# Kernel optimization log

Hardware: AMD Instinct MI355X
Metric: run time of the kernel (lower is better)

The kernel has to match this reference:

```python
import jax, jax.numpy as jnp
import numpy as np

N = 200000; S = 128; P = 4; K = 27
C_IN = 256; C_OUT = 256; N_IN = 64; N_OUT = 64
DILATIONS = [1, 3, 9, 27]
EPS = 1e-5


def _build_pairs():
    """Precompute (in_idx, out_idx) gather/scatter pairs per path & kernel offset,
    mimicking MinkowskiEngine's coordinate-hash-map kernel maps."""
    rng = np.random.default_rng(0)
    lin = rng.choice(S ** 3, size=N, replace=False)
    xs = lin // (S * S); ys = (lin // S) % S; zs = lin % S
    coords = np.stack([xs, ys, zs], axis=1).astype(np.int64)  # [N,3]
    order = np.argsort(lin)
    skeys = lin[order]
    offs = np.array([[dx, dy, dz] for dx in (-1, 0, 1) for dy in (-1, 0, 1) for dz in (-1, 0, 1)], dtype=np.int64)  # [27,3]
    pairs = [[None] * K for _ in range(P)]
    max_m = 1
    for p, d in enumerate(DILATIONS):
        for k in range(K):
            nc = coords + offs[k] * d  # neighbor coords for each output point
            valid = np.all((nc >= 0) & (nc < S), axis=1)
            idx_out = np.nonzero(valid)[0]
            nkey = (nc[valid, 0] * S + nc[valid, 1]) * S + nc[valid, 2]
            pos = np.searchsorted(skeys, nkey)
            pos_c = np.minimum(pos, N - 1)
            found = skeys[pos_c] == nkey
            j = order[pos_c[found]]       # source (input) point index
            i = idx_out[found]            # destination (output) point index
            pairs[p][k] = (j.astype(np.int32), i.astype(np.int32))
            max_m = max(max_m, len(j))
    in_idx = np.full((P, K, max_m), N, dtype=np.int32)   # sentinel N -> zero/dummy row
    out_idx = np.full((P, K, max_m), N, dtype=np.int32)
    for p in range(P):
        for k in range(K):
            j, i = pairs[p][k]
            in_idx[p, k, : len(j)] = j
            out_idx[p, k, : len(i)] = i
    return jnp.asarray(in_idx), jnp.asarray(out_idx)


def setup_inputs() -> dict:
    key = jax.random.key(0)
    ks = jax.random.split(key, 8)
    in_idx, out_idx = _build_pairs()
    x = jax.random.normal(ks[0], (N, C_IN), dtype=jnp.float32)
    Wl = jax.random.normal(ks[1], (P, C_IN, N_IN), dtype=jnp.float32) * (1.0 / np.sqrt(C_IN))
    bl = jax.random.normal(ks[2], (P, N_IN), dtype=jnp.float32) * 0.01
    Wc = jax.random.normal(ks[3], (P, K, N_IN, N_OUT), dtype=jnp.float32) * (1.0 / np.sqrt(K * N_IN))
    gamma = jnp.ones((P, N_OUT), dtype=jnp.float32)
    beta = jnp.zeros((P, N_OUT), dtype=jnp.float32)
    W2 = jax.random.normal(ks[4], (C_OUT, C_OUT), dtype=jnp.float32) * (1.0 / np.sqrt(C_OUT))
    b2 = jax.random.normal(ks[5], (C_OUT,), dtype=jnp.float32) * 0.01
    return {"x": x, "Wl": Wl, "bl": bl, "Wc": Wc, "gamma": gamma, "beta": beta,
            "W2": W2, "b2": b2, "in_idx": in_idx, "out_idx": out_idx}


def reference(x, Wl, bl, Wc, gamma, beta, W2, b2, in_idx, out_idx):
    n = x.shape[0]
    zero_row = jnp.zeros((1, N_IN), dtype=x.dtype)
    paths = []
    for p in range(P):  # fixed small cardinality loop (structurally distinct dilations)
        h = x @ Wl[p] + bl[p]                      # MinkowskiLinear: [N, nIn]
        hp = jnp.concatenate([h, zero_row], axis=0)  # dummy row for padded pairs
        g = hp[in_idx[p]]                          # gather: [K, M, nIn]
        c = jnp.einsum('kmc,kcd->kmd', g, Wc[p])   # per-offset matmul
        out = jnp.zeros((n + 1, N_OUT), dtype=x.dtype)
        out = out.at[out_idx[p].reshape(-1)].add(c.reshape(-1, N_OUT))[:n]  # scatter-add
        mu = out.mean(axis=0)
        var = jnp.mean((out - mu) ** 2, axis=0)    # biased var, as torch BN training mode
        out = (out - mu) * jax.lax.rsqrt(var + EPS) * gamma[p] + beta[p]
        paths.append(jax.nn.relu(out))
    cat = jnp.concatenate(paths, axis=-1)          # [N, out_features]
    return cat @ W2 + b2 + x                       # 1x1 linear + identity residual
```

## Files before the change

kernel.cpp:

```cpp
#include <hip/hip_runtime.h>
#include <hip/hip_bf16.h>

constexpr float EPS = 1e-5f;

typedef _Float16 f16x8 __attribute__((ext_vector_type(8)));
typedef __attribute__((ext_vector_type(4))) float floatx4;

__global__ __launch_bounds__(256) void k0_wct(
    const float* __restrict__ Wc, _Float16* __restrict__ wct)
{
    __shared__ float T[64][65];
    const int pk = blockIdx.x;
    const float* src = Wc + (size_t)pk * 4096;
    _Float16* dst = wct + (size_t)pk * 4096;
    const int t = threadIdx.x;
    #pragma unroll
    for (int e = 0; e < 16; e++) {
        const int idx = t + 256 * e;
        T[idx >> 6][idx & 63] = src[idx];
    }
    __syncthreads();
    #pragma unroll
    for (int e = 0; e < 16; e++) {
        const int idx = t + 256 * e;
        const int d = idx >> 6, q = idx & 63;
        const int sc = q >> 3, j = q & 7;
        const int cin = ((sc ^ (d & 7)) << 3) | j;
        dst[idx] = (_Float16)T[cin][d];
    }
}

__global__ __launch_bounds__(256) void k0_wlt(
    const float* __restrict__ Wl, _Float16* __restrict__ wlt)
{
    __shared__ float T[64][65];
    const int p = blockIdx.x, ct = blockIdx.y;
    const int t = threadIdx.x;
    #pragma unroll
    for (int e = 0; e < 16; e++) {
        const int idx = t + 256 * e;
        const int c = idx >> 6, d = idx & 63;
        T[c][d] = Wl[((size_t)p * 256 + ct * 64 + c) * 64 + d];
    }
    __syncthreads();
    #pragma unroll
    for (int e = 0; e < 16; e++) {
        const int idx = t + 256 * e;
        const int d = idx >> 6, c = idx & 63;
        wlt[((size_t)p * 64 + d) * 256 + ct * 64 + c] = (_Float16)T[c][d];
    }
}

__global__ __launch_bounds__(256) void k0_w2t(
    const float* __restrict__ W2, _Float16* __restrict__ w2t)
{
    __shared__ float T[64][65];
    const int kt = blockIdx.x, ct = blockIdx.y;
    const int t = threadIdx.x;
    #pragma unroll
    for (int e = 0; e < 16; e++) {
        const int idx = t + 256 * e;
        const int kk = idx >> 6, c = idx & 63;
        T[kk][c] = W2[((size_t)kt * 64 + kk) * 256 + ct * 64 + c];
    }
    __syncthreads();
    #pragma unroll
    for (int e = 0; e < 16; e++) {
        const int idx = t + 256 * e;
        const int c = idx >> 6, kk = idx & 63;
        w2t[((size_t)ct * 64 + c) * 256 + kt * 64 + kk] = (_Float16)T[kk][c];
    }
}

__global__ __launch_bounds__(512, 4) void k1_gemm_h(
    const float* __restrict__ x, const _Float16* __restrict__ wlt,
    const float* __restrict__ bl, _Float16* __restrict__ hb, int n)
{
    __shared__ __align__(16) _Float16 As[128 * 128];
    __shared__ __align__(16) _Float16 Bs[64 * 128];
    __shared__ float blS[256];

    const int row0 = blockIdx.x << 7;
    const int t    = threadIdx.x;
    const int lane = t & 63;
    const int wv   = t >> 6;
    const int mrow = lane & 15;
    const int quad = lane >> 4;

    if (t < 256) blS[t] = bl[t];

    floatx4 acc[4][4];
    #pragma unroll
    for (int a = 0; a < 4; a++)
        #pragma unroll
        for (int b = 0; b < 4; b++) acc[a][b] = floatx4{0.f, 0.f, 0.f, 0.f};

    #pragma unroll
    for (int kh = 0; kh < 2; kh++) {
        __syncthreads();
        #pragma unroll
        for (int i = 0; i < 4; i++) {
            const int cid = t + 512 * i;
            const int r = cid >> 4, ck = cid & 15;
            const int gr = row0 + r;
            f16x8 v;
            if (gr < n) {
                const float* g = x + (size_t)gr * 256 + kh * 128 + (ck << 3);
                const float4 f0 = *(const float4*)g;
                const float4 f1 = *(const float4*)(g + 4);
                v[0] = (_Float16)f0.x; v[1] = (_Float16)f0.y;
                v[2] = (_Float16)f0.z; v[3] = (_Float16)f0.w;
                v[4] = (_Float16)f1.x; v[5] = (_Float16)f1.y;
                v[6] = (_Float16)f1.z; v[7] = (_Float16)f1.w;
            } else {
                #pragma unroll
                for (int j = 0; j < 8; j++) v[j] = (_Float16)0.f;
            }
            *(f16x8*)&As[r * 128 + ((ck ^ (r & 7)) << 3)] = v;
        }
        #pragma unroll
        for (int cg = 0; cg < 4; cg++) {
            __syncthreads();
            #pragma unroll
            for (int it = 0; it < 2; it++) {
                const int lin = t + 512 * it;
                const int r = lin >> 4, sc = lin & 15;
                const _Float16* gs = wlt + (size_t)(cg * 64 + r) * 256
                                     + kh * 128 + ((sc ^ (r & 7)) << 3);
                __builtin_amdgcn_global_load_lds(
                    (const __attribute__((address_space(1))) void*)gs,
                    (__attribute__((address_space(3))) void*)((char*)Bs + lin * 16),
                    16, 0, 0);
            }
            __syncthreads();
            #pragma unroll
            for (int s = 0; s < 4; s++) {
                const int r = (wv << 4) + mrow;
                const f16x8 a = *(const f16x8*)&As[r * 128 + ((((s << 2) + quad) ^ (r & 7)) << 3)];
                #pragma unroll
                for (int tc = 0; tc < 4; tc++) {
                    const int rn = (tc << 4) + mrow;
                    const f16x8 b = *(const f16x8*)&Bs[rn * 128 + ((((s << 2) + quad) ^ (rn & 7)) << 3)];
                    acc[cg][tc] = __builtin_amdgcn_mfma_f32_16x16x32_f16(a, b, acc[cg][tc], 0, 0, 0);
                }
            }
        }
    }
    __syncthreads();
    #pragma unroll
    for (int cg = 0; cg < 4; cg++)
        #pragma unroll
        for (int tc = 0; tc < 4; tc++)
            #pragma unroll
            for (int rg = 0; rg < 4; rg++) {
                const int r = row0 + (wv << 4) + (quad << 2) + rg;
                const int c = (cg << 6) + (tc << 4) + mrow;
                if (r < n)
                    hb[(size_t)r * 256 + c] = (_Float16)(acc[cg][tc][rg] + blS[c]);
            }
}

__global__ __launch_bounds__(512) void k2_conv(
    const _Float16* __restrict__ hb, const _Float16* __restrict__ wct,
    const int* __restrict__ in_idx, const int* __restrict__ out_idx,
    float* __restrict__ accum, float* __restrict__ ssum,
    float* __restrict__ ssq, int n, int M)
{
    __shared__ __align__(16) _Float16 Ws[2][4096];
    __shared__ float Acc[128][66];
    __shared__ int csrc[2][128];
    __shared__ int cdst[2][128];
    __shared__ int spos_s[27];
    __shared__ int epos_s[27];

    const int p    = blockIdx.y;
    const int t    = threadIdx.x;
    const int lane = t & 63;
    const int wv   = t >> 6;
    const int mrow = lane & 15;
    const int quad = lane >> 4;

    const int nwg = gridDim.x;
    const int qq = nwg >> 3, rr = nwg & 7;
    const int xcd = blockIdx.x & 7, ii = blockIdx.x >> 3;
    const int bx = (xcd < rr ? xcd * (qq + 1) : rr * (qq + 1) + (xcd - rr) * qq) + ii;
    const int row0 = bx << 7;

    for (int i = t; i < 128 * 66; i += 512) ((float*)Acc)[i] = 0.0f;

    if (t < 54) {
        const int kk = (t < 27) ? t : t - 27;
        const int upper = (row0 + 128 > n) ? n : row0 + 128;
        const int target = (t < 27) ? row0 : upper;
        const int* oi = out_idx + (size_t)(p * 27 + kk) * M;
        int lo = 0, hi = M;
        while (lo < hi) {
            const int mid = (lo + hi) >> 1;
            if (oi[mid] < target) lo = mid + 1; else hi = mid;
        }
        if (t < 27) spos_s[kk] = lo; else epos_s[kk] = lo;
    }
    __syncthreads();

#define STAGE(buf, kk) do {                                                         \
        const char* gs_ = (const char*)wct + (((size_t)(p * 27 + (kk))) << 13)      \
                          + (wv << 10) + (lane << 4);                               \
        __builtin_amdgcn_global_load_lds(                                           \
            (const __attribute__((address_space(1))) void*)gs_,                     \
            (__attribute__((address_space(3))) void*)((char*)&Ws[buf][0] + (wv << 10)), \
            16, 0, 0);                                                              \
    } while (0)

#define COMPACT(buf, kk) do {                                                       \
        if (t < 128) {                                                              \
            const int sp_ = spos_s[kk];                                             \
            int cn_ = epos_s[kk] - sp_;                                             \
            if (cn_ > 128) cn_ = 128;                                               \
            const size_t base_ = (size_t)(p * 27 + (kk)) * M + sp_;                 \
            int v_ = n;                                                             \
            if (t < cn_) {                                                          \
                v_ = in_idx[base_ + t];                                             \
                cdst[buf][t] = out_idx[base_ + t] - row0;                           \
            }                                                                       \
            csrc[buf][t] = v_;                                                      \
        }                                                                           \
    } while (0)

    STAGE(0, 0);
    COMPACT(0, 0);
    __syncthreads();

    for (int k = 0; k < 27; k++) {
        const int cur = k & 1;
        if (k < 26) { STAGE(cur ^ 1, k + 1); COMPACT(cur ^ 1, k + 1); }

        int cnt = epos_s[k] - spos_s[k];
        if (cnt > 128) cnt = 128;
        const int tids = ((cnt + 15) >> 4) << 2;
        const int bsw  = (quad ^ (mrow & 7)) << 3;

        for (int tid = wv; tid < tids; tid += 8) {
            const int tr = tid >> 2, tc = tid & 3;
            const int srow = csrc[cur][(tr << 4) + mrow];
            const _Float16* ar = hb + ((size_t)srow << 8) + (p << 6) + (quad << 3);
            const f16x8 a0 = *(const f16x8*)ar;
            const f16x8 a1 = *(const f16x8*)(ar + 32);
            const int brow = ((tc << 4) + mrow) << 6;
            const f16x8 b0 = *(const f16x8*)(Ws[cur] + brow + bsw);
            const f16x8 b1 = *(const f16x8*)(Ws[cur] + brow + (bsw ^ 32));
            floatx4 c = {0.f, 0.f, 0.f, 0.f};
            c = __builtin_amdgcn_mfma_f32_16x16x32_f16(a0, b0, c, 0, 0, 0);
            c = __builtin_amdgcn_mfma_f32_16x16x32_f16(a1, b1, c, 0, 0, 0);
            #pragma unroll
            for (int rg = 0; rg < 4; rg++) {
                const int m = (tr << 4) + (quad << 2) + rg;
                if (m < cnt)
                    Acc[cdst[cur][m]][(tc << 4) + mrow] += c[rg];
            }
        }
        __syncthreads();
    }

    {
        const int col = t & 63;
        float s = 0.f, s2 = 0.f;
        for (int r = wv; r < 128; r += 8) {
            const float v = Acc[r][col];
            s += v; s2 += v * v;
        }
        float* red = (float*)&Ws[0][0];
        red[wv * 64 + col] = s;
        red[512 + wv * 64 + col] = s2;
        __syncthreads();
        if (t < 64) {
            float a = 0.f, b = 0.f;
            #pragma unroll
            for (int w = 0; w < 8; w++) {
                a += red[w * 64 + t];
                b += red[512 + w * 64 + t];
            }
            atomicAdd(&ssum[(p << 6) + t], a);
            atomicAdd(&ssq[(p << 6) + t], b);
        }
    }

    for (int i = t; i < 128 * 32; i += 512) {
        const int r = i >> 5, cc = (i & 31) << 1;
        const int gr = row0 + r;
        if (gr < n)
            *(float2*)(accum + (size_t)gr * 256 + (p << 6) + cc) =
                *(const float2*)&Acc[r][cc];
    }
#undef STAGE
#undef COMPACT
}

__global__ void k3_final(
    const float* __restrict__ ssum, const float* __restrict__ ssq,
    const float* __restrict__ gamma, const float* __restrict__ beta,
    float* __restrict__ scale, float* __restrict__ shift, int n)
{
    const int t = threadIdx.x;
    const float inv_n = 1.0f / (float)n;
    const float mu  = ssum[t] * inv_n;
    const float var = ssq[t] * inv_n - mu * mu;
    const float sc  = gamma[t] * rsqrtf(var + EPS);
    scale[t] = sc;
    shift[t] = beta[t] - mu * sc;
}

__global__ __launch_bounds__(512, 4) void k4_gemm_out(
    float* __restrict__ io, const _Float16* __restrict__ w2t,
    const float* __restrict__ b2, const float* __restrict__ x,
    const float* __restrict__ scale, const float* __restrict__ shift, int n)
{
    __shared__ __align__(16) _Float16 As[128 * 128];
    __shared__ __align__(16) _Float16 Bs[64 * 128];
    __shared__ float scS[256], shS[256], b2S[256];

    const int row0 = blockIdx.x << 7;
    const int t    = threadIdx.x;
    const int lane = t & 63;
    const int wv   = t >> 6;
    const int mrow = lane & 15;
    const int quad = lane >> 4;

    if (t < 256) { scS[t] = scale[t]; shS[t] = shift[t]; b2S[t] = b2[t]; }

    floatx4 acc[4][4];
    #pragma unroll
    for (int a = 0; a < 4; a++)
        #pragma unroll
        for (int b = 0; b < 4; b++) acc[a][b] = floatx4{0.f, 0.f, 0.f, 0.f};

    #pragma unroll
    for (int kh = 0; kh < 2; kh++) {
        __syncthreads();
        #pragma unroll
        for (int i = 0; i < 4; i++) {
            const int cid = t + 512 * i;
            const int r = cid >> 4, ck = cid & 15;
            const int gr = row0 + r;
            const int kg = kh * 128 + (ck << 3);
            f16x8 v;
            if (gr < n) {
                const float* g = io + (size_t)gr * 256 + kg;
                const float4 f0 = *(const float4*)g;
                const float4 f1 = *(const float4*)(g + 4);
                float f[8] = {f0.x, f0.y, f0.z, f0.w, f1.x, f1.y, f1.z, f1.w};
                #pragma unroll
                for (int j = 0; j < 8; j++)
                    v[j] = (_Float16)fmaxf(f[j] * scS[kg + j] + shS[kg + j], 0.f);
            } else {
                #pragma unroll
                for (int j = 0; j < 8; j++) v[j] = (_Float16)0.f;
            }
            *(f16x8*)&As[r * 128 + ((ck ^ (r & 7)) << 3)] = v;
        }
        #pragma unroll
        for (int cg = 0; cg < 4; cg++) {
            __syncthreads();
            #pragma unroll
            for (int it = 0; it < 2; it++) {
                const int lin = t + 512 * it;
                const int r = lin >> 4, sc = lin & 15;
                const _Float16* gs = w2t + (size_t)(cg * 64 + r) * 256
                                     + kh * 128 + ((sc ^ (r & 7)) << 3);
                __builtin_amdgcn_global_load_lds(
                    (const __attribute__((address_space(1))) void*)gs,
                    (__attribute__((address_space(3))) void*)((char*)Bs + lin * 16),
                    16, 0, 0);
            }
            __syncthreads();
            #pragma unroll
            for (int s = 0; s < 4; s++) {
                const int r = (wv << 4) + mrow;
                const f16x8 a = *(const f16x8*)&As[r * 128 + ((((s << 2) + quad) ^ (r & 7)) << 3)];
                #pragma unroll
                for (int tc = 0; tc < 4; tc++) {
                    const int rn = (tc << 4) + mrow;
                    const f16x8 b = *(const f16x8*)&Bs[rn * 128 + ((((s << 2) + quad) ^ (rn & 7)) << 3)];
                    acc[cg][tc] = __builtin_amdgcn_mfma_f32_16x16x32_f16(a, b, acc[cg][tc], 0, 0, 0);
                }
            }
        }
    }
    __syncthreads();
    #pragma unroll
    for (int cg = 0; cg < 4; cg++)
        #pragma unroll
        for (int tc = 0; tc < 4; tc++)
            #pragma unroll
            for (int rg = 0; rg < 4; rg++) {
                const int r = row0 + (wv << 4) + (quad << 2) + rg;
                const int c = (cg << 6) + (tc << 4) + mrow;
                if (r < n)
                    io[(size_t)r * 256 + c] = acc[cg][tc][rg] + b2S[c] + x[(size_t)r * 256 + c];
            }
}

extern "C" void kernel_launch(void* const* d_in, const int* in_sizes, int n_in,
                              void* d_out, int out_size, void* d_ws, size_t ws_size,
                              hipStream_t stream)
{
    const float* x     = (const float*)d_in[0];
    const float* Wl    = (const float*)d_in[1];
    const float* bl    = (const float*)d_in[2];
    const float* Wc    = (const float*)d_in[3];
    const float* gamma = (const float*)d_in[4];
    const float* beta  = (const float*)d_in[5];
    const float* W2    = (const float*)d_in[6];
    const float* b2    = (const float*)d_in[7];
    const int* in_idx  = (const int*)d_in[8];
    const int* out_idx = (const int*)d_in[9];

    const int n = in_sizes[0] / 256;
    const int M = in_sizes[8] / (4 * 27);

    float* accum = (float*)d_out;

    _Float16* hb = (_Float16*)d_ws;
    const size_t hb_bytes = (size_t)(n + 1) * 256 * sizeof(_Float16);
    _Float16* wct = (_Float16*)((char*)d_ws + hb_bytes);
    const size_t wct_bytes = (size_t)4 * 27 * 4096 * sizeof(_Float16);
    _Float16* wlt = (_Float16*)((char*)wct + wct_bytes);
    _Float16* w2t = (_Float16*)((char*)wlt + 256 * 256 * sizeof(_Float16));
    float* stats = (float*)((char*)w2t + 256 * 256 * sizeof(_Float16));
    float* ssum = stats, *ssq = stats + 256;
    float* scalev = stats + 512, *shiftv = stats + 768;

    hipMemsetAsync(stats, 0, 512 * sizeof(float), stream);
    hipMemsetAsync(hb + (size_t)n * 256, 0, 256 * sizeof(_Float16), stream);

    k0_wct<<<dim3(108), 256, 0, stream>>>(Wc, wct);
    k0_wlt<<<dim3(4, 4), 256, 0, stream>>>(Wl, wlt);
    k0_w2t<<<dim3(4, 4), 256, 0, stream>>>(W2, w2t);

    const int rb2 = (n + 127) >> 7;

    k1_gemm_h<<<rb2, 512, 0, stream>>>(x, wlt, bl, hb, n);

    dim3 g2(rb2, 4);
    k2_conv<<<g2, 512, 0, stream>>>(hb, wct, in_idx, out_idx, accum, ssum, ssq, n, M);

    k3_final<<<1, 256, 0, stream>>>(ssum, ssq, gamma, beta, scalev, shiftv, n);

    k4_gemm_out<<<rb2, 512, 0, stream>>>(accum, w2t, b2, x, scalev, shiftv, n);
}
```

Before: 1.135 ms.

## Make sparse conv output-stationary with register accumulation; double-buffer GEMM weight tiles

The conv kernel no longer scatter-adds MFMA results into a shared-memory accumulator through compacted source and destination lists. Each 128-row output tile now builds, per kernel offset, a dense source-row table indexed by output row, using a four-slot ring tagged with the offset index. It gathers one hb row per output row and accumulates all 27 offsets in MFMA registers, prefetching the next offset's gather and index data one or two steps ahead. BN statistics are reduced with wave shuffles, and the bulky Acc LDS buffer is removed, which allows a stated occupancy of 4 blocks. The two dense GEMM kernels double-buffer the weight tile loaded via global_load_lds so one __syncthreads per stage is dropped. This relies on implicit wait counts before barriers.

Measured after the change: 1.002 ms. 11.7% less time.

```diff
diff --git a/kernel.cpp b/kernel.cpp
--- a/kernel.cpp
+++ b/kernel.cpp
@@ -77,7 +77,7 @@
     const float* __restrict__ bl, _Float16* __restrict__ hb, int n)
 {
     __shared__ __align__(16) _Float16 As[128 * 128];
-    __shared__ __align__(16) _Float16 Bs[64 * 128];
+    __shared__ __align__(16) _Float16 Bs[2][64 * 128];
     __shared__ float blS[256];
 
     const int row0 = blockIdx.x << 7;
@@ -87,7 +87,24 @@
     const int mrow = lane & 15;
     const int quad = lane >> 4;
 
+#define STAGE_B1(buf_, st_) do {                                                \
+        const int kh_ = (st_) >> 2, cg_ = (st_) & 3;                            \
+        _Pragma("unroll")                                                       \
+        for (int it = 0; it < 2; it++) {                                        \
+            const int lin = t + 512 * it;                                       \
+            const int r = lin >> 4, sc = lin & 15;                              \
+            const _Float16* gs = wlt + (size_t)(cg_ * 64 + r) * 256             \
+                                 + kh_ * 128 + ((sc ^ (r & 7)) << 3);           \
+            __builtin_amdgcn_global_load_lds(                                   \
+                (const __attribute__((address_space(1))) void*)gs,              \
+                (__attribute__((address_space(3))) void*)                       \
+                    ((char*)&Bs[buf_][0] + lin * 16),                           \
+                16, 0, 0);                                                      \
+        }                                                                       \
+    } while (0)
+
     if (t < 256) blS[t] = bl[t];
+    STAGE_B1(0, 0);
 
     floatx4 acc[4][4];
     #pragma unroll
@@ -120,19 +137,17 @@
         }
         #pragma unroll
         for (int cg = 0; cg < 4; cg++) {
+            const int st = kh * 4 + cg;
             __syncthreads();
-            #pragma unroll
-            for (int it = 0; it < 2; it++) {
-                const int lin = t + 512 * it;
-                const int r = lin >> 4, sc = lin & 15;
-                const _Float16* gs = wlt + (size_t)(cg * 64 + r) * 256
-                                     + kh * 128 + ((sc ^ (r & 7)) << 3);
-                __builtin_amdgcn_global_load_lds(
-                    (const __attribute__((address_space(1))) void*)gs,
-                    (__attribute__((address_space(3))) void*)((char*)Bs + lin * 16),
-                    16, 0, 0);
-            }
-            __syncthreads();
+            if (st < 7) {
+                if (st == 0) STAGE_B1(1, 1);
+                else if (st == 1) STAGE_B1(0, 2);
+                else if (st == 2) STAGE_B1(1, 3);
+                else if (st == 3) STAGE_B1(0, 4);
+                else if (st == 4) STAGE_B1(1, 5);
+                else if (st == 5) STAGE_B1(0, 6);
+                else              STAGE_B1(1, 7);
+            }
             #pragma unroll
             for (int s = 0; s < 4; s++) {
                 const int r = (wv << 4) + mrow;
@@ -140,13 +155,12 @@
                 #pragma unroll
                 for (int tc = 0; tc < 4; tc++) {
                     const int rn = (tc << 4) + mrow;
-                    const f16x8 b = *(const f16x8*)&Bs[rn * 128 + ((((s << 2) + quad) ^ (rn & 7)) << 3)];
+                    const f16x8 b = *(const f16x8*)&Bs[st & 1][rn * 128 + ((((s << 2) + quad) ^ (rn & 7)) << 3)];
                     acc[cg][tc] = __builtin_amdgcn_mfma_f32_16x16x32_f16(a, b, acc[cg][tc], 0, 0, 0);
                 }
             }
         }
     }
-    __syncthreads();
     #pragma unroll
     for (int cg = 0; cg < 4; cg++)
         #pragma unroll
@@ -158,20 +172,21 @@
                 if (r < n)
                     hb[(size_t)r * 256 + c] = (_Float16)(acc[cg][tc][rg] + blS[c]);
             }
-}
-
-__global__ __launch_bounds__(512) void k2_conv(
+#undef STAGE_B1
+}
+
+__global__ __launch_bounds__(512, 4) void k2_conv(
     const _Float16* __restrict__ hb, const _Float16* __restrict__ wct,
     const int* __restrict__ in_idx, const int* __restrict__ out_idx,
     float* __restrict__ accum, float* __restrict__ ssum,
     float* __restrict__ ssq, int n, int M)
 {
     __shared__ __align__(16) _Float16 Ws[2][4096];
-    __shared__ float Acc[128][66];
-    __shared__ int csrc[2][128];
-    __shared__ int cdst[2][128];
+    __shared__ int src2[4][128];
     __shared__ int spos_s[27];
     __shared__ int epos_s[27];
+    __shared__ float redS[8][64];
+    __shared__ float redQ[8][64];
 
     const int p    = blockIdx.y;
     const int t    = threadIdx.x;
@@ -186,7 +201,7 @@
     const int bx = (xcd < rr ? xcd * (qq + 1) : rr * (qq + 1) + (xcd - rr) * qq) + ii;
     const int row0 = bx << 7;
 
-    for (int i = t; i < 128 * 66; i += 512) ((float*)Acc)[i] = 0.0f;
+    const int SENT = 31 << 19;
 
     if (t < 54) {
         const int kk = (t < 27) ? t : t - 27;
@@ -200,99 +215,124 @@
         }
         if (t < 27) spos_s[kk] = lo; else epos_s[kk] = lo;
     }
+    if (t < 128) {
+        src2[0][t] = SENT; src2[1][t] = SENT;
+        src2[2][t] = SENT; src2[3][t] = SENT;
+    }
     __syncthreads();
 
 #define STAGE(buf, kk) do {                                                         \
         const char* gs_ = (const char*)wct + (((size_t)(p * 27 + (kk))) << 13)      \
-                          + (wv << 10) + (lane << 4);                               \
+                          + (t << 4);                                               \
         __builtin_amdgcn_global_load_lds(                                           \
             (const __attribute__((address_space(1))) void*)gs_,                     \
-            (__attribute__((address_space(3))) void*)((char*)&Ws[buf][0] + (wv << 10)), \
+            (__attribute__((address_space(3))) void*)((char*)&Ws[buf][0] + (t << 4)), \
             16, 0, 0);                                                              \
     } while (0)
 
-#define COMPACT(buf, kk) do {                                                       \
-        if (t < 128) {                                                              \
-            const int sp_ = spos_s[kk];                                             \
-            int cn_ = epos_s[kk] - sp_;                                             \
-            if (cn_ > 128) cn_ = 128;                                               \
-            const size_t base_ = (size_t)(p * 27 + (kk)) * M + sp_;                 \
-            int v_ = n;                                                             \
-            if (t < cn_) {                                                          \
-                v_ = in_idx[base_ + t];                                             \
-                cdst[buf][t] = out_idx[base_ + t] - row0;                           \
-            }                                                                       \
-            csrc[buf][t] = v_;                                                      \
-        }                                                                           \
-    } while (0)
-
+    int ivS = 0, ovS = 0, cntS = 0;
+    if (t < 128) {
+        #pragma unroll
+        for (int K = 0; K < 2; K++) {
+            int c = epos_s[K] - spos_s[K];
+            if (c > 128) c = 128;
+            if (t < c) {
+                const size_t b = (size_t)(p * 27 + K) * M + spos_s[K] + t;
+                src2[K][out_idx[b] - row0] = (K << 19) | in_idx[b];
+            }
+        }
+        cntS = epos_s[2] - spos_s[2];
+        if (cntS > 128) cntS = 128;
+        if (t < cntS) {
+            const size_t b = (size_t)(p * 27 + 2) * M + spos_s[2] + t;
+            ivS = in_idx[b]; ovS = out_idx[b];
+        }
+    }
     STAGE(0, 0);
-    COMPACT(0, 0);
-    __syncthreads();
+    __syncthreads();
+
+    const int arow = (wv << 4) + mrow;
+    const int bsw  = (quad ^ (mrow & 7)) << 3;
+
+    f16x8 g0a, g0b, g1a, g1b;
+    {
+        const int v = src2[0][arow];
+        const int src = ((v >> 19) == 0) ? (v & 0x7FFFF) : n;
+        const _Float16* ar = hb + ((size_t)src << 8) + (p << 6) + (quad << 3);
+        g0a = *(const f16x8*)ar;
+        g0b = *(const f16x8*)(ar + 32);
+    }
+
+    floatx4 acc[4];
+    #pragma unroll
+    for (int tc = 0; tc < 4; tc++) acc[tc] = floatx4{0.f, 0.f, 0.f, 0.f};
 
     for (int k = 0; k < 27; k++) {
-        const int cur = k & 1;
-        if (k < 26) { STAGE(cur ^ 1, k + 1); COMPACT(cur ^ 1, k + 1); }
-
-        int cnt = epos_s[k] - spos_s[k];
-        if (cnt > 128) cnt = 128;
-        const int tids = ((cnt + 15) >> 4) << 2;
-        const int bsw  = (quad ^ (mrow & 7)) << 3;
-
-        for (int tid = wv; tid < tids; tid += 8) {
-            const int tr = tid >> 2, tc = tid & 3;
-            const int srow = csrc[cur][(tr << 4) + mrow];
-            const _Float16* ar = hb + ((size_t)srow << 8) + (p << 6) + (quad << 3);
-            const f16x8 a0 = *(const f16x8*)ar;
-            const f16x8 a1 = *(const f16x8*)(ar + 32);
+        if (k < 26) {
+            const int v = src2[(k + 1) & 3][arow];
+            const int src = ((v >> 19) == (k + 1)) ? (v & 0x7FFFF) : n;
+            const _Float16* ar = hb + ((size_t)src << 8) + (p << 6) + (quad << 3);
+            g1a = *(const f16x8*)ar;
+            g1b = *(const f16x8*)(ar + 32);
+        }
+        if (k < 25 && t < cntS)
+            src2[(k + 2) & 3][ovS - row0] = ((k + 2) << 19) | ivS;
+        int ivN = 0, ovN = 0, cntN = 0;
+        if (k < 24 && t < 128) {
+            cntN = epos_s[k + 3] - spos_s[k + 3];
+            if (cntN > 128) cntN = 128;
+            if (t < cntN) {
+                const size_t b = (size_t)(p * 27 + k + 3) * M + spos_s[k + 3] + t;
+                ivN = in_idx[b]; ovN = out_idx[b];
+            }
+        }
+        if (k < 26) STAGE((k + 1) & 1, k + 1);
+        #pragma unroll
+        for (int tc = 0; tc < 4; tc++) {
             const int brow = ((tc << 4) + mrow) << 6;
-            const f16x8 b0 = *(const f16x8*)(Ws[cur] + brow + bsw);
-            const f16x8 b1 = *(const f16x8*)(Ws[cur] + brow + (bsw ^ 32));
-            floatx4 c = {0.f, 0.f, 0.f, 0.f};
-            c = __builtin_amdgcn_mfma_f32_16x16x32_f16(a0, b0, c, 0, 0, 0);
-            c = __builtin_amdgcn_mfma_f32_16x16x32_f16(a1, b1, c, 0, 0, 0);
-            #pragma unroll
-            for (int rg = 0; rg < 4; rg++) {
-                const int m = (tr << 4) + (quad << 2) + rg;
-                if (m < cnt)
-                    Acc[cdst[cur][m]][(tc << 4) + mrow] += c[rg];
-            }
+            const f16x8 b0 = *(const f16x8*)(Ws[k & 1] + brow + bsw);
+            const f16x8 b1 = *(const f16x8*)(Ws[k & 1] + brow + (bsw ^ 32));
+            acc[tc] = __builtin_amdgcn_mfma_f32_16x16x32_f16(g0a, b0, acc[tc], 0, 0, 0);
+            acc[tc] = __builtin_amdgcn_mfma_f32_16x16x32_f16(g0b, b1, acc[tc], 0, 0, 0);
         }
         __syncthreads();
-    }
-
-    {
-        const int col = t & 63;
-        float s = 0.f, s2 = 0.f;
-        for (int r = wv; r < 128; r += 8) {
-            const float v = Acc[r][col];
-            s += v; s2 += v * v;
-        }
-        float* red = (float*)&Ws[0][0];
-        red[wv * 64 + col] = s;
-        red[512 + wv * 64 + col] = s2;
-        __syncthreads();
-        if (t < 64) {
-            float a = 0.f, b = 0.f;
-            #pragma unroll
-            for (int w = 0; w < 8; w++) {
-                a += red[w * 64 + t];
-                b += red[512 + w * 64 + t];
-            }
-            atomicAdd(&ssum[(p << 6) + t], a);
-            atomicAdd(&ssq[(p << 6) + t], b);
-        }
-    }
-
-    for (int i = t; i < 128 * 32; i += 512) {
-        const int r = i >> 5, cc = (i & 31) << 1;
-        const int gr = row0 + r;
-        if (gr < n)
-            *(float2*)(accum + (size_t)gr * 256 + (p << 6) + cc) =
-                *(const float2*)&Acc[r][cc];
-    }
+        g0a = g1a; g0b = g1b;
+        ivS = ivN; ovS = ovN; cntS = cntN;
+    }
+
+    #pragma unroll
+    for (int tc = 0; tc < 4; tc++) {
+        float s = 0.f, q = 0.f;
+        #pragma unroll
+        for (int rg = 0; rg < 4; rg++) {
+            const float v = acc[tc][rg];
+            s += v; q += v * v;
+        }
+        s += __shfl_xor(s, 16); s += __shfl_xor(s, 32);
+        q += __shfl_xor(q, 16); q += __shfl_xor(q, 32);
+        if (quad == 0) {
+            redS[wv][(tc << 4) + mrow] = s;
+            redQ[wv][(tc << 4) + mrow] = q;
+        }
+    }
+    __syncthreads();
+    if (t < 64) {
+        float a = 0.f, b = 0.f;
+        #pragma unroll
+        for (int w = 0; w < 8; w++) { a += redS[w][t]; b += redQ[w][t]; }
+        atomicAdd(&ssum[(p << 6) + t], a);
+        atomicAdd(&ssq[(p << 6) + t], b);
+    }
+
+    #pragma unroll
+    for (int tc = 0; tc < 4; tc++)
+        #pragma unroll
+        for (int rg = 0; rg < 4; rg++) {
+            const int r = row0 + (wv << 4) + (quad << 2) + rg;
+            if (r < n)
+                accum[(size_t)r * 256 + (p << 6) + (tc << 4) + mrow] = acc[tc][rg];
+        }
 #undef STAGE
-#undef COMPACT
 }
 
 __global__ void k3_final(
@@ -315,7 +355,7 @@
     const float* __restrict__ scale, const float* __restrict__ shift, int n)
 {
     __shared__ __align__(16) _Float16 As[128 * 128];
-    __shared__ __align__(16) _Float16 Bs[64 * 128];
+    __shared__ __align__(16) _Float16 Bs[2][64 * 128];
     __shared__ float scS[256], shS[256], b2S[256];
 
     const int row0 = blockIdx.x << 7;
@@ -325,7 +365,24 @@
     const int mrow = lane & 15;
     const int quad = lane >> 4;
 
+#define STAGE_B4(buf_, st_) do {                                                \
+        const int kh_ = (st_) >> 2, cg_ = (st_) & 3;                            \
+        _Pragma("unroll")                                                       \
+        for (int it = 0; it < 2; it++) {                                        \
+            const int lin = t + 512 * it;                                       \
+            const int r = lin >> 4, sc = lin & 15;                              \
+            const _Float16* gs = w2t + (size_t)(cg_ * 64 + r) * 256             \
+                                 + kh_ * 128 + ((sc ^ (r & 7)) << 3);           \
+            __builtin_amdgcn_global_load_lds(                                   \
+                (const __attribute__((address_space(1))) void*)gs,              \
+                (__attribute__((address_space(3))) void*)                       \
+                    ((char*)&Bs[buf_][0] + lin * 16),                           \
+                16, 0, 0);                                                      \
+        }                                                                       \
+    } while (0)
+
     if (t < 256) { scS[t] = scale[t]; shS[t] = shift[t]; b2S[t] = b2[t]; }
+    STAGE_B4(0, 0);
 
     floatx4 acc[4][4];
     #pragma unroll
@@ -359,19 +416,17 @@
         }
         #pragma unroll
         for (int cg = 0; cg < 4; cg++) {
+            const int st = kh * 4 + cg;
             __syncthreads();
-            #pragma unroll
-            for (int it = 0; it < 2; it++) {
-                const int lin = t + 512 * it;
-                const int r = lin >> 4, sc = lin & 15;
-                const _Float16* gs = w2t + (size_t)(cg * 64 + r) * 256
-                                     + kh * 128 + ((sc ^ (r & 7)) << 3);
-                __builtin_amdgcn_global_load_lds(
-                    (const __attribute__((address_space(1))) void*)gs,
-                    (__attribute__((address_space(3))) void*)((char*)Bs + lin * 16),
-                    16, 0, 0);
-            }
-            __syncthreads();
+            if (st < 7) {
+                if (st == 0) STAGE_B4(1, 1);
+                else if (st == 1) STAGE_B4(0, 2);
+                else if (st == 2) STAGE_B4(1, 3);
+                else if (st == 3) STAGE_B4(0, 4);
+                else if (st == 4) STAGE_B4(1, 5);
+                else if (st == 5) STAGE_B4(0, 6);
+                else              STAGE_B4(1, 7);
+            }
             #pragma unroll
             for (int s = 0; s < 4; s++) {
                 const int r = (wv << 4) + mrow;
@@ -379,7 +434,7 @@
                 #pragma unroll
                 for (int tc = 0; tc < 4; tc++) {
                     const int rn = (tc << 4) + mrow;
-                    const f16x8 b = *(const f16x8*)&Bs[rn * 128 + ((((s << 2) + quad) ^ (rn & 7)) << 3)];
+                    const f16x8 b = *(const f16x8*)&Bs[st & 1][rn * 128 + ((((s << 2) + quad) ^ (rn & 7)) << 3)];
                     acc[cg][tc] = __builtin_amdgcn_mfma_f32_16x16x32_f16(a, b, acc[cg][tc], 0, 0, 0);
                 }
             }
@@ -397,6 +452,7 @@
                 if (r < n)
                     io[(size_t)r * 256 + c] = acc[cg][tc][rg] + b2S[c] + x[(size_t)r * 256 + c];
             }
+#undef STAGE_B4
 }
 
 extern "C" void kernel_launch(void* const* d_in, const int* in_sizes, int n_in,
```
